# Kernel optimization log

Measured on AMD Instinct MI355X. Metric: run time of the kernel, lower is better.

The kernel has to match this reference:

```python
import jax, jax.numpy as jnp
import numpy as np

NX, NY = 512, 512
NT = 240
STRIDE = 4
H = 1e-3
DT = 5e-8
F0 = 100000.0
T0 = 6e-6
AMP = 1.0
GAUSS_A = 5e6
RHO = 1600.0
C_INIT = dict(C11=1e11, C22=1e10, C12=8e9, C16=2.5e10, C26=3e9, C66=1.2e10)
C_LO, C_HI = 1e9, 1e13


def setup_inputs() -> dict:
    # Ricker wavelet source signal (full time resolution)
    t = np.arange(NT) * DT
    tau = t - T0
    pf = (np.pi * F0 * tau) ** 2
    signal = (AMP * (1.0 - 2.0 * pf) * np.exp(-pf)).astype(np.float32)
    # Gaussian point-load spatial distribution centered at (0,0)
    Lx, Ly = H * (NX - 1), H * (NY - 1)
    x = np.linspace(-Lx / 2, Lx / 2, NX, dtype=np.float64)
    y = np.linspace(-Ly / 2, Ly / 2, NY, dtype=np.float64)
    X, Y = np.meshgrid(x, y, indexing='ij')
    r2 = X ** 2 + Y ** 2
    gauss = (GAUSS_A / np.pi * np.exp(-GAUSS_A * r2)).astype(np.float32)
    return {
        'log_C11': jnp.array([np.log(C_INIT['C11'])], dtype=jnp.float32),
        'log_C22': jnp.array([np.log(C_INIT['C22'])], dtype=jnp.float32),
        'log_C12': jnp.array([np.log(C_INIT['C12'])], dtype=jnp.float32),
        'log_C16': jnp.array([np.log(C_INIT['C16'])], dtype=jnp.float32),
        'log_C26': jnp.array([np.log(C_INIT['C26'])], dtype=jnp.float32),
        'log_C66': jnp.array([np.log(C_INIT['C66'])], dtype=jnp.float32),
        'rho': jnp.array([RHO], dtype=jnp.float32),
        'source_signal': jnp.asarray(signal),
        'gaussian_dist': jnp.asarray(gauss),
    }


def _stencils(u, h_inv_sq):
    # u: (B, nx, ny), zero-padded 3x3 FD stencils (conv2d_fixed equivalent)
    p = jnp.pad(u, ((0, 0), (1, 1), (1, 1)))
    dxx = (p[:, 2:, 1:-1] + p[:, :-2, 1:-1] - 2.0 * u) * h_inv_sq
    dyy = (p[:, 1:-1, 2:] + p[:, 1:-1, :-2] - 2.0 * u) * h_inv_sq
    dxy = 0.25 * (p[:, :-2, :-2] - p[:, :-2, 2:] - p[:, 2:, :-2] + p[:, 2:, 2:]) * h_inv_sq
    return dxx, dyy, dxy


def _simulate(log_Cs, rho, source_signal, gaussian_dist):
    log_C11, log_C22, log_C12, log_C16, log_C26, log_C66 = log_Cs
    C11 = jnp.clip(jnp.exp(log_C11[0]), C_LO, C_HI)
    C22 = jnp.clip(jnp.exp(log_C22[0]), C_LO, C_HI)
    C12 = jnp.clip(jnp.exp(log_C12[0]), C_LO, C_HI)
    C16 = jnp.clip(jnp.exp(log_C16[0]), C_LO, C_HI)
    C26 = jnp.clip(jnp.exp(log_C26[0]), C_LO, C_HI)
    C66 = jnp.clip(jnp.exp(log_C66[0]), C_LO, C_HI)
    r = rho[0]
    h_inv_sq = jnp.float32(1.0 / (H * H))
    dt2 = jnp.float32(DT * DT)
    g = gaussian_dist[None]  # (1, nx, ny)
    zeros = jnp.zeros((1, NX, NY), dtype=jnp.float32)

    def step(carry, f_amp):
        ux1, uy1, ux2, uy2 = carry
        # source on y component
        force_y = f_amp * g
        dxx_ux, dyy_ux, dxy_ux = _stencils(ux1, h_inv_sq)
        dxx_uy, dyy_uy, dxy_uy = _stencils(uy1, h_inv_sq)
        Lux = (C11 * dxx_ux + C66 * dyy_ux + (C12 + C66) * dxy_uy
               + 2.0 * C16 * dxy_ux + C16 * dxx_uy + C26 * dyy_uy) / r
        Luy = (C66 * dxx_uy + C22 * dyy_uy + (C12 + C66) * dxy_ux
               + C16 * dxx_ux + C26 * dyy_ux + 2.0 * C26 * dxy_uy + force_y) / r
        ux_new = 2.0 * ux1 - ux2 + dt2 * Lux
        uy_new = 2.0 * uy1 - uy2 + dt2 * Luy
        return (ux_new, uy_new, ux1, uy1), (ux_new, uy_new)

    init = (zeros, zeros, zeros, zeros)
    _, (ux_hist, uy_hist) = jax.lax.scan(step, init, source_signal)
    # (nt, 1, nx, ny) -> (1, nt, nx, ny), then PRIMARY time stride subsample
    ux_fields = jnp.moveaxis(ux_hist, 0, 1)[:, ::STRIDE]
    uy_fields = jnp.moveaxis(uy_hist, 0, 1)[:, ::STRIDE]
    return ux_fields, uy_fields


def reference(log_C11, log_C22, log_C12, log_C16, log_C26, log_C66, rho, source_signal, gaussian_dist):
    return _simulate((log_C11, log_C22, log_C12, log_C16, log_C26, log_C66),
                     rho, source_signal, gaussian_dist)
```

## Files before the change

kernel.cpp:

```cpp
#include <hip/hip_runtime.h>

#define NXg    512
#define Sg     262144
#define NFRg   60
#define Kg     12
#define NCHUNK 20
#define Tg     32
#define Eg     56
#define EJP    58
#define NSEGR  14
#define NTHR   896
#define NPAIR  (Eg * (Eg / 2))

__global__ __launch_bounds__(512)
void cfrp_init(float4* __restrict__ ws4)
{
    const int gt = (int)blockIdx.x * 512 + (int)threadIdx.x;
    ws4[gt] = make_float4(0.f, 0.f, 0.f, 0.f);
}

#define CELLSTEP(nv, NW, N, NE, Wt, C, Et, SW, S, SE, P, GF)                 \
{                                                                            \
    const float sxx_x = N.x + S.x - 2.0f * C.x;                              \
    const float syy_x = Wt.x + Et.x - 2.0f * C.x;                            \
    const float sxy_x = 0.25f * (NW.x - NE.x - SW.x + SE.x);                 \
    const float sxx_y = N.y + S.y - 2.0f * C.y;                              \
    const float syy_y = Wt.y + Et.y - 2.0f * C.y;                            \
    const float sxy_y = 0.25f * (NW.y - NE.y - SW.y + SE.y);                 \
    const float lux = kc11 * sxx_x + kc66 * syy_x + kc1266 * sxy_y           \
                    + kc16x2 * sxy_x + kc16 * sxx_y + kc26 * syy_y;          \
    const float luy = kc66 * sxx_y + kc22 * syy_y + kc1266 * sxy_x           \
                    + kc16 * sxx_x + kc26 * syy_x + kc26x2 * sxy_y           \
                    + fa * GF;                                               \
    nv = make_float2(2.0f * C.x - P.x + lux, 2.0f * C.y - P.y + luy);        \
}

__global__ __launch_bounds__(NTHR)
void cfrp_chunk(const float* __restrict__ lc11, const float* __restrict__ lc22,
                const float* __restrict__ lc12, const float* __restrict__ lc16,
                const float* __restrict__ lc26, const float* __restrict__ lc66,
                const float* __restrict__ rho_p, const float* __restrict__ sig,
                const float* __restrict__ gauss, float* __restrict__ out,
                const float2* __restrict__ gcur, const float2* __restrict__ gprev,
                float2* __restrict__ ncur, float2* __restrict__ nprev,
                int TB)
{
    __shared__ float2 sf[2][Eg * EJP];

    const int tid = (int)threadIdx.x;
    const int w  = (int)blockIdx.x;
    const int q  = w & 7;
    const int r_ = w >> 3;
    const int ti = q * 2 + (r_ >> 4);
    const int tj = r_ & 15;
    const int oi = ti * Tg - Kg;
    const int oj = tj * Tg - Kg;

    const float C11 = fminf(fmaxf(expf(lc11[0]), 1e9f), 1e13f);
    const float C22 = fminf(fmaxf(expf(lc22[0]), 1e9f), 1e13f);
    const float C12 = fminf(fmaxf(expf(lc12[0]), 1e9f), 1e13f);
    const float C16 = fminf(fmaxf(expf(lc16[0]), 1e9f), 1e13f);
    const float C26 = fminf(fmaxf(expf(lc26[0]), 1e9f), 1e13f);
    const float C66 = fminf(fmaxf(expf(lc66[0]), 1e9f), 1e13f);
    const float rh   = rho_p[0];
    const float dt2  = 2.5e-15f;
    const float kk   = dt2 * 1e6f / rh;
    const float kc11 = kk * C11, kc22 = kk * C22, kc66 = kk * C66;
    const float kc16 = kk * C16, kc26 = kk * C26;
    const float kc1266 = kk * (C12 + C66);
    const float kc16x2 = 2.0f * kc16;
    const float kc26x2 = 2.0f * kc26;
    const float gsc = dt2 / rh;

    #pragma unroll
    for (int s = 0; s < 2; ++s) {
        const int p = tid + s * NTHR;
        if (p < NPAIR) {
            const int rr  = p / (Eg / 2);
            const int cc2 = (p - rr * (Eg / 2)) * 2;
            const int gi  = oi + rr;
            const int gj  = oj + cc2;
            float4 v = make_float4(0.f, 0.f, 0.f, 0.f);
            if (((unsigned)gi < NXg) && ((unsigned)gj < NXg))
                v = *(const float4*)&gcur[gi * NXg + gj];
            const int d = rr * EJP + cc2;
            *(float4*)&sf[0][d] = v;
            *(float4*)&sf[1][d] = v;
        }
    }
    if (tid < Eg) {
        const int d = tid * EJP + Eg;
        *(float4*)&sf[0][d] = make_float4(0.f, 0.f, 0.f, 0.f);
        *(float4*)&sf[1][d] = make_float4(0.f, 0.f, 0.f, 0.f);
    }

    const int  srow = tid >> 4;
    const int  scol = tid & 15;
    const bool act  = (scol < NSEGR) && (srow >= 1) && (srow <= Eg - 2);
    const int  c0   = scol * 4;
    const int  gi   = oi + srow;
    const int  gj0  = oj + c0;
    const int  dC   = srow * EJP + c0;
    const bool in4  = ((unsigned)gi < NXg) && (gj0 >= 0) && (gj0 < (int)NXg);
    const bool own  = act && (srow >= Kg) && (srow < Kg + Tg)
                          && (scol >= 3) && (scol <= 10);
    const int  go0  = gi * NXg + gj0;

    float2 pv0 = {0,0}, pv1 = {0,0}, pv2 = {0,0}, pv3 = {0,0};
    float  gf0 = 0.f, gf1 = 0.f, gf2 = 0.f, gf3 = 0.f;
    if (act && in4) {
        const float4 t0 = *(const float4*)&gprev[go0];
        const float4 t1 = *(const float4*)&gprev[go0 + 2];
        pv0 = make_float2(t0.x, t0.y); pv1 = make_float2(t0.z, t0.w);
        pv2 = make_float2(t1.x, t1.y); pv3 = make_float2(t1.z, t1.w);
        const float4 g = *(const float4*)&gauss[go0];
        gf0 = g.x * gsc; gf1 = g.y * gsc; gf2 = g.z * gsc; gf3 = g.w * gsc;
    }
    __syncthreads();

    float2 cv0, cv1, cv2, cv3;
    {
        const float4 a = *(const float4*)&sf[0][dC];
        const float4 b = *(const float4*)&sf[0][dC + 2];
        cv0 = make_float2(a.x, a.y); cv1 = make_float2(a.z, a.w);
        cv2 = make_float2(b.x, b.y); cv3 = make_float2(b.z, b.w);
    }

    const float2* cur = sf[0];
    float2*       nxt = sf[1];

    #pragma unroll
    for (int st = 0; st < Kg; ++st) {
        const float fa = sig[TB + st];
        if (act) {
            const int iT = dC - EJP;
            const int iB = dC + EJP;
            const float4 t01 = *(const float4*)&cur[iT];
            const float4 t23 = *(const float4*)&cur[iT + 2];
            const float2 twv = cur[iT - 1];
            const float2 tev = cur[iT + 4];
            const float4 b01 = *(const float4*)&cur[iB];
            const float4 b23 = *(const float4*)&cur[iB + 2];
            const float2 bwv = cur[iB - 1];
            const float2 bev = cur[iB + 4];
            const float2 wmv = cur[dC - 1];
            const float2 emv = cur[dC + 4];

            const float2 ta0 = twv, ta1 = make_float2(t01.x, t01.y),
                         ta2 = make_float2(t01.z, t01.w),
                         ta3 = make_float2(t23.x, t23.y),
                         ta4 = make_float2(t23.z, t23.w), ta5 = tev;
            const float2 ba0 = bwv, ba1 = make_float2(b01.x, b01.y),
                         ba2 = make_float2(b01.z, b01.w),
                         ba3 = make_float2(b23.x, b23.y),
                         ba4 = make_float2(b23.z, b23.w), ba5 = bev;

            float2 nv0, nv1, nv2, nv3;
            CELLSTEP(nv0, ta0, ta1, ta2, wmv, cv0, cv1, ba0, ba1, ba2, pv0, gf0)
            CELLSTEP(nv1, ta1, ta2, ta3, cv0, cv1, cv2, ba1, ba2, ba3, pv1, gf1)
            CELLSTEP(nv2, ta2, ta3, ta4, cv1, cv2, cv3, ba2, ba3, ba4, pv2, gf2)
            CELLSTEP(nv3, ta3, ta4, ta5, cv2, cv3, emv, ba3, ba4, ba5, pv3, gf3)

            if (!in4) {
                nv0 = nv1 = nv2 = nv3 = make_float2(0.f, 0.f);
            }
            pv0 = cv0; pv1 = cv1; pv2 = cv2; pv3 = cv3;
            cv0 = nv0; cv1 = nv1; cv2 = nv2; cv3 = nv3;

            *(float4*)&nxt[dC]     = make_float4(cv0.x, cv0.y, cv1.x, cv1.y);
            *(float4*)&nxt[dC + 2] = make_float4(cv2.x, cv2.y, cv3.x, cv3.y);

            if (((st & 3) == 0) && own) {
                const int fr = (TB + st) >> 2;
                *(float4*)&out[fr * Sg + go0] =
                    make_float4(cv0.x, cv1.x, cv2.x, cv3.x);
                *(float4*)&out[(fr + NFRg) * Sg + go0] =
                    make_float4(cv0.y, cv1.y, cv2.y, cv3.y);
            }
        }
        __syncthreads();
        float2* tmp = (float2*)cur; cur = nxt; nxt = tmp;
    }

    if (own) {
        *(float4*)&ncur[go0]      = make_float4(cv0.x, cv0.y, cv1.x, cv1.y);
        *(float4*)&ncur[go0 + 2]  = make_float4(cv2.x, cv2.y, cv3.x, cv3.y);
        *(float4*)&nprev[go0]     = make_float4(pv0.x, pv0.y, pv1.x, pv1.y);
        *(float4*)&nprev[go0 + 2] = make_float4(pv2.x, pv2.y, pv3.x, pv3.y);
    }
}

extern "C" void kernel_launch(void* const* d_in, const int* in_sizes, int n_in,
                              void* d_out, int out_size, void* d_ws, size_t ws_size,
                              hipStream_t stream) {
    const float* lc11  = (const float*)d_in[0];
    const float* lc22  = (const float*)d_in[1];
    const float* lc12  = (const float*)d_in[2];
    const float* lc16  = (const float*)d_in[3];
    const float* lc26  = (const float*)d_in[4];
    const float* lc66  = (const float*)d_in[5];
    const float* rho_p = (const float*)d_in[6];
    const float* sig   = (const float*)d_in[7];
    const float* gauss = (const float*)d_in[8];
    float* out  = (float*)d_out;
    float2* ws2 = (float2*)d_ws;

    float2* Ac = ws2;           float2* Ap = ws2 + Sg;
    float2* Bc = ws2 + 2 * Sg;  float2* Bp = ws2 + 3 * Sg;

    hipLaunchKernelGGL(cfrp_init, dim3(512), dim3(512), 0, stream, (float4*)d_ws);

    for (int c = 0; c < NCHUNK; ++c) {
        float2 *rc, *rp, *wc, *wp;
        if (c & 1) { rc = Bc; rp = Bp; wc = Ac; wp = Ap; }
        else       { rc = Ac; rp = Ap; wc = Bc; wp = Bp; }
        hipLaunchKernelGGL(cfrp_chunk, dim3(256), dim3(NTHR), 0, stream,
                           lc11, lc22, lc12, lc16, lc26, lc66, rho_p, sig,
                           gauss, out, rc, rp, wc, wp, c * Kg);
    }
}
```

Before: 684.1 us.

## Replace block barriers with neighbor-wave flag sync and shrink temporal tile

Each step's __syncthreads is replaced by per-wave LDS flags. A wave waits only for the waves above and below it to finish the previous step before reading the shared stencil buffer. The temporal blocking depth drops from 12 to 8 steps, so the tile edge shrinks from 56 to 48 and the block from 896 to 576 threads, each row now mapped exactly onto 12 lanes. This cuts redundant halo computation and the cost of block-wide barriers, at the price of more chunk launches and re-reads of global state, spin-wait overhead, and a correctness dependency on the neighbor-only ordering argument.

Measured after the change: 548.5 us. 1.25x faster.

```diff
diff --git a/kernel.cpp b/kernel.cpp
--- a/kernel.cpp
+++ b/kernel.cpp
@@ -3,14 +3,14 @@
 #define NXg    512
 #define Sg     262144
 #define NFRg   60
-#define Kg     12
-#define NCHUNK 20
+#define Kg     8
+#define NCHUNK 30
 #define Tg     32
-#define Eg     56
-#define EJP    58
-#define NSEGR  14
-#define NTHR   896
-#define NPAIR  (Eg * (Eg / 2))
+#define Eg     48
+#define EJP    50
+#define NSEGR  12
+#define NTHR   576
+#define NWAVE  9
 
 __global__ __launch_bounds__(512)
 void cfrp_init(float4* __restrict__ ws4)
@@ -46,8 +46,10 @@
                 int TB)
 {
     __shared__ float2 sf[2][Eg * EJP];
+    __shared__ int sflag[NWAVE * 16];
 
     const int tid = (int)threadIdx.x;
+    const int wv  = tid >> 6;
     const int w  = (int)blockIdx.x;
     const int q  = w & 7;
     const int r_ = w >> 3;
@@ -74,36 +76,34 @@
 
     #pragma unroll
     for (int s = 0; s < 2; ++s) {
-        const int p = tid + s * NTHR;
-        if (p < NPAIR) {
-            const int rr  = p / (Eg / 2);
-            const int cc2 = (p - rr * (Eg / 2)) * 2;
-            const int gi  = oi + rr;
-            const int gj  = oj + cc2;
-            float4 v = make_float4(0.f, 0.f, 0.f, 0.f);
-            if (((unsigned)gi < NXg) && ((unsigned)gj < NXg))
-                v = *(const float4*)&gcur[gi * NXg + gj];
-            const int d = rr * EJP + cc2;
-            *(float4*)&sf[0][d] = v;
-            *(float4*)&sf[1][d] = v;
-        }
+        const int p  = tid + s * NTHR;
+        const int rr = p / 24;
+        const int cp = (p - rr * 24) * 2;
+        const int gi = oi + rr;
+        const int gj = oj + cp;
+        float4 v = make_float4(0.f, 0.f, 0.f, 0.f);
+        if (((unsigned)gi < NXg) && ((unsigned)gj < NXg))
+            v = *(const float4*)&gcur[gi * NXg + gj];
+        const int li = rr * EJP + cp;
+        *(float4*)&sf[0][li] = v;
+        *(float4*)&sf[1][li] = v;
     }
     if (tid < Eg) {
-        const int d = tid * EJP + Eg;
-        *(float4*)&sf[0][d] = make_float4(0.f, 0.f, 0.f, 0.f);
-        *(float4*)&sf[1][d] = make_float4(0.f, 0.f, 0.f, 0.f);
-    }
-
-    const int  srow = tid >> 4;
-    const int  scol = tid & 15;
-    const bool act  = (scol < NSEGR) && (srow >= 1) && (srow <= Eg - 2);
+        const int li = tid * EJP + Eg;
+        *(float4*)&sf[0][li] = make_float4(0.f, 0.f, 0.f, 0.f);
+        *(float4*)&sf[1][li] = make_float4(0.f, 0.f, 0.f, 0.f);
+    }
+    if (tid < NWAVE) sflag[tid * 16] = 0;
+
+    const int  srow = tid / NSEGR;
+    const int  scol = tid - srow * NSEGR;
+    const bool act  = (srow >= 1) && (srow <= Eg - 2);
     const int  c0   = scol * 4;
     const int  gi   = oi + srow;
     const int  gj0  = oj + c0;
     const int  dC   = srow * EJP + c0;
     const bool in4  = ((unsigned)gi < NXg) && (gj0 >= 0) && (gj0 < (int)NXg);
-    const bool own  = act && (srow >= Kg) && (srow < Kg + Tg)
-                          && (scol >= 3) && (scol <= 10);
+    const bool own  = (srow >= Kg) && (srow < Kg + Tg) && (scol >= 2) && (scol <= 9);
     const int  go0  = gi * NXg + gj0;
 
     float2 pv0 = {0,0}, pv1 = {0,0}, pv2 = {0,0}, pv3 = {0,0};
@@ -131,6 +131,21 @@
 
     #pragma unroll
     for (int st = 0; st < Kg; ++st) {
+        if (st > 0) {
+            if (wv > 0) {
+                while (__hip_atomic_load(&sflag[(wv - 1) * 16],
+                                         __ATOMIC_ACQUIRE,
+                                         __HIP_MEMORY_SCOPE_WORKGROUP) < st)
+                    __builtin_amdgcn_s_sleep(1);
+            }
+            if (wv < NWAVE - 1) {
+                while (__hip_atomic_load(&sflag[(wv + 1) * 16],
+                                         __ATOMIC_ACQUIRE,
+                                         __HIP_MEMORY_SCOPE_WORKGROUP) < st)
+                    __builtin_amdgcn_s_sleep(1);
+            }
+        }
+
         const float fa = sig[TB + st];
         if (act) {
             const int iT = dC - EJP;
@@ -178,7 +193,10 @@
                     make_float4(cv0.y, cv1.y, cv2.y, cv3.y);
             }
         }
-        __syncthreads();
+        if ((tid & 63) == 0) {
+            __hip_atomic_store(&sflag[wv * 16], st + 1,
+                               __ATOMIC_RELEASE, __HIP_MEMORY_SCOPE_WORKGROUP);
+        }
         float2* tmp = (float2*)cur; cur = nxt; nxt = tmp;
     }
 
```
